# Kernel tuning notes

Hardware: AMD Instinct MI355X
Metric: run time of the kernel (lower is better)

The kernel has to match this reference:

```python
import jax, jax.numpy as jnp
import numpy as np
from jax import lax

B, T, D, H, L = 2048, 512, 64, 16, 10
LOG2PI = float(np.log(2.0 * np.pi))


def _gru_cell(x, h, Wih, Whh, bih, bhh):
    # torch GRUCell gate order: r, z, n
    gi = x @ Wih.T + bih
    gh = h @ Whh.T + bhh
    ir, iz, inn = jnp.split(gi, 3, axis=-1)
    hr, hz, hn = jnp.split(gh, 3, axis=-1)
    r = jax.nn.sigmoid(ir + hr)
    z = jax.nn.sigmoid(iz + hz)
    n = jnp.tanh(inn + r * hn)
    return (1.0 - z) * n + z * h


def _mlp_head(h, W1, b1, W2, b2, Wmu, bmu, Wcov, bcov):
    hh = jax.nn.relu(h @ W1.T + b1)
    hh = jax.nn.relu(hh @ W2.T + b2)
    mu = hh @ Wmu.T + bmu
    sigma = jnp.exp(hh @ Wcov.T + bcov)
    return mu, sigma


def setup_inputs():
    key = jax.random.key(0)
    ks = jax.random.split(key, 24)

    def he(k, shape, fan_in):
        return jax.random.normal(k, shape, dtype=jnp.float32) * np.float32(np.sqrt(2.0 / fan_in))

    z = lambda *s: jnp.zeros(s, jnp.float32)
    p = {}
    p['x'] = jax.random.normal(ks[0], (B, T, D), dtype=jnp.float32)
    p['eps'] = jax.random.normal(ks[1], (B, T, L), dtype=jnp.float32)
    # bidirectional inference GRU
    p['bi_Wih_f'] = he(ks[2], (3 * H, D), D); p['bi_Whh_f'] = he(ks[3], (3 * H, H), H)
    p['bi_bih_f'] = z(3 * H); p['bi_bhh_f'] = z(3 * H)
    p['bi_Wih_b'] = he(ks[4], (3 * H, D), D); p['bi_Whh_b'] = he(ks[5], (3 * H, H), H)
    p['bi_bih_b'] = z(3 * H); p['bi_bhh_b'] = z(3 * H)
    # inference GRUCell on [z_prev, context]
    p['infz_Wih'] = he(ks[6], (3 * H, L + 2 * H), L + 2 * H); p['infz_Whh'] = he(ks[7], (3 * H, H), H)
    p['infz_bih'] = z(3 * H); p['infz_bhh'] = z(3 * H)
    # inference MLP
    p['inf_W1'] = he(ks[8], (H, H), H); p['inf_b1'] = z(H)
    p['inf_W2'] = he(ks[9], (H, H), H); p['inf_b2'] = z(H)
    p['inf_Wmu'] = he(ks[10], (L, H), H); p['inf_bmu'] = z(L)
    p['inf_Wcov'] = he(ks[11], (L, H), H); p['inf_bcov'] = z(L)
    # generative prior GRUCell + MLP (frozen in torch)
    p['genz_Wih'] = he(ks[12], (3 * H, L), L); p['genz_Whh'] = he(ks[13], (3 * H, H), H)
    p['genz_bih'] = z(3 * H); p['genz_bhh'] = z(3 * H)
    p['genzmlp_W1'] = he(ks[14], (H, H), H); p['genzmlp_b1'] = z(H)
    p['genzmlp_W2'] = he(ks[15], (H, H), H); p['genzmlp_b2'] = z(H)
    p['genzmlp_Wmu'] = he(ks[16], (L, H), H); p['genzmlp_bmu'] = z(L)
    p['genzmlp_Wcov'] = he(ks[17], (L, H), H); p['genzmlp_bcov'] = z(L)
    # generative emission GRUCell + MLP (outputs 3*D)
    p['genr_Wih'] = he(ks[18], (3 * H, L), L); p['genr_Whh'] = he(ks[19], (3 * H, H), H)
    p['genr_bih'] = z(3 * H); p['genr_bhh'] = z(3 * H)
    p['genr_W1'] = he(ks[20], (H, H), H); p['genr_b1'] = z(H)
    p['genr_W2'] = he(ks[21], (3 * D, H), H); p['genr_b2'] = z(3 * D)
    return p


def _forward(x, eps, bi_Wih_f, bi_Whh_f, bi_bih_f, bi_bhh_f, bi_Wih_b, bi_Whh_b, bi_bih_b, bi_bhh_b,
             infz_Wih, infz_Whh, infz_bih, infz_bhh,
             inf_W1, inf_b1, inf_W2, inf_b2, inf_Wmu, inf_bmu, inf_Wcov, inf_bcov,
             genz_Wih, genz_Whh, genz_bih, genz_bhh,
             genzmlp_W1, genzmlp_b1, genzmlp_W2, genzmlp_b2, genzmlp_Wmu, genzmlp_bmu, genzmlp_Wcov, genzmlp_bcov,
             genr_Wih, genr_Whh, genr_bih, genr_bhh, genr_W1, genr_b1, genr_W2, genr_b2):
    b, t, d = x.shape
    xt = jnp.transpose(x, (1, 0, 2))      # [T, B, D] time-major
    eps_t = jnp.transpose(eps, (1, 0, 2))  # [T, B, L]
    h0 = jnp.zeros((b, H), x.dtype)

    def fstep(h, xin):
        h2 = _gru_cell(xin, h, bi_Wih_f, bi_Whh_f, bi_bih_f, bi_bhh_f)
        return h2, h2

    def bstep(h, xin):
        h2 = _gru_cell(xin, h, bi_Wih_b, bi_Whh_b, bi_bih_b, bi_bhh_b)
        return h2, h2

    _, fwd = lax.scan(fstep, h0, xt)               # [T, B, H]
    _, bwd_rev = lax.scan(bstep, h0, xt[::-1])
    bwd = bwd_rev[::-1]                            # [T, B, H]

    pad = jnp.zeros((1, b, H), x.dtype)
    h_right = jnp.concatenate([pad, fwd[:-1]], axis=0)   # h^{->}_{t-1}
    h_left = jnp.concatenate([bwd[1:], pad], axis=0)     # h^{<-}_{t+1}
    ctx = jnp.concatenate([h_right, h_left], axis=-1)    # [T, B, 2H]

    def step(carry, inp):
        h_z, h_gz, h_gr, z_prev = carry
        c, e, xi = inp
        h_z = _gru_cell(jnp.concatenate([z_prev, c], axis=-1), h_z, infz_Wih, infz_Whh, infz_bih, infz_bhh)
        q_mu, q_sig = _mlp_head(h_z, inf_W1, inf_b1, inf_W2, inf_b2, inf_Wmu, inf_bmu, inf_Wcov, inf_bcov)
        h_gz = _gru_cell(z_prev, h_gz, genz_Wih, genz_Whh, genz_bih, genz_bhh)
        p_mu, p_sig = _mlp_head(h_gz, genzmlp_W1, genzmlp_b1, genzmlp_W2, genzmlp_b2, genzmlp_Wmu, genzmlp_bmu, genzmlp_Wcov, genzmlp_bcov)
        # KL(N(q_mu,q_sig) || N(p_mu,p_sig))
        kl = jnp.log(p_sig / q_sig) + (q_sig * q_sig + (q_mu - p_mu) ** 2) / (2.0 * p_sig * p_sig) - 0.5
        kl_t = kl.sum(axis=-1).mean()
        z_t = q_mu + q_sig * e  # rsample
        h_gr = _gru_cell(z_t, h_gr, genr_Wih, genr_Whh, genr_bih, genr_bhh)
        r = jax.nn.relu(h_gr @ genr_W1.T + genr_b1) @ genr_W2.T + genr_b2  # [B, 3D]
        r_mu = r[:, :d]
        r_diag = jnp.exp(r[:, d:2 * d]) + 1e-4
        w = r[:, 2 * d:]  # rank-1 cov factor
        # LowRankMVN log_prob via Woodbury (rank 1): Cov = D + w w^T
        delta = xi - r_mu
        dinv = 1.0 / r_diag
        wd = w * dinv
        cap = 1.0 + jnp.sum(wd * w, axis=-1)  # capacitance
        maha = jnp.sum(delta * delta * dinv, axis=-1) - jnp.sum(wd * delta, axis=-1) ** 2 / cap
        logdet = jnp.sum(jnp.log(r_diag), axis=-1) + jnp.log(cap)
        logp = -0.5 * (d * LOG2PI + logdet + maha)
        nll_t = -logp.mean()
        return (h_z, h_gz, h_gr, z_t), (kl_t, nll_t)

    z0 = jnp.zeros((b, L), x.dtype)
    carry0 = (h0, h0, h0, z0)
    _, (kls, nlls) = lax.scan(step, carry0, (ctx, eps_t, xt))
    return nlls.sum(), kls.sum()


def reference(x, eps, bi_Wih_f, bi_Whh_f, bi_bih_f, bi_bhh_f, bi_Wih_b, bi_Whh_b, bi_bih_b, bi_bhh_b,
              infz_Wih, infz_Whh, infz_bih, infz_bhh,
              inf_W1, inf_b1, inf_W2, inf_b2, inf_Wmu, inf_bmu, inf_Wcov, inf_bcov,
              genz_Wih, genz_Whh, genz_bih, genz_bhh,
              genzmlp_W1, genzmlp_b1, genzmlp_W2, genzmlp_b2, genzmlp_Wmu, genzmlp_bmu, genzmlp_Wcov, genzmlp_bcov,
              genr_Wih, genr_Whh, genr_bih, genr_bhh, genr_W1, genr_b1, genr_W2, genr_b2):
    return _forward(x, eps, bi_Wih_f, bi_Whh_f, bi_bih_f, bi_bhh_f, bi_Wih_b, bi_Whh_b, bi_bih_b, bi_bhh_b,
                    infz_Wih, infz_Whh, infz_bih, infz_bhh,
                    inf_W1, inf_b1, inf_W2, inf_b2, inf_Wmu, inf_bmu, inf_Wcov, inf_bcov,
                    genz_Wih, genz_Whh, genz_bih, genz_bhh,
                    genzmlp_W1, genzmlp_b1, genzmlp_W2, genzmlp_b2, genzmlp_Wmu, genzmlp_bmu, genzmlp_Wcov, genzmlp_bcov,
                    genr_Wih, genr_Whh, genr_bih, genr_bhh, genr_W1, genr_b1, genr_W2, genr_b2)
```

## Files before the change

### kernel.cpp

```cpp
#include <hip/hip_runtime.h>

namespace {

typedef __attribute__((ext_vector_type(4))) _Float16 half4v;
typedef __attribute__((ext_vector_type(4))) float   float4v;
typedef unsigned int u32;

#define MFMA16(a,b,c) __builtin_amdgcn_mfma_f32_16x16x16f16((a),(b),(c),0,0,0)

constexpr int Bb = 2048;
constexpr int Tt = 512;
constexpr float LOG2PI_ = 1.8378770664093453f;

struct InPtrs { const float* p[42]; };

__device__ __forceinline__ float rcpf(float x){ return __builtin_amdgcn_rcpf(x); }
__device__ __forceinline__ float sigm(float x){ return rcpf(1.0f + __expf(-x)); }
__device__ __forceinline__ float tanh_(float x){ return 1.0f - 2.0f*rcpf(1.0f + __expf(2.0f*x)); }

__device__ __forceinline__ void barrier_lds(){
  asm volatile("s_waitcnt lgkmcnt(0)" ::: "memory");
  __builtin_amdgcn_s_barrier();
  asm volatile("" ::: "memory");
}

__global__ void zero2(float* out){ if (threadIdx.x < 2) out[threadIdx.x] = 0.f; }

__device__ __forceinline__ void gru_update(const float4v& Dr, const float4v& Dz,
                                           const float4v& Dn, const float4v& Dh, half4v& hB){
  #pragma unroll
  for (int i = 0; i < 4; ++i){
    const float rr = sigm(Dr[i]);
    const float zz = sigm(Dz[i]);
    const float nn = tanh_(Dn[i] + rr*Dh[i]);
    const float hp = (float)hB[i];
    hB[i] = (_Float16)(nn + zz*(hp - nn));
  }
}

__device__ __forceinline__ half4v relu_pack(const float4v& D){
  half4v o;
  #pragma unroll
  for (int i = 0; i < 4; ++i) o[i] = (_Float16)fmaxf(D[i], 0.f);
  return o;
}

constexpr int CH = 8;
constexpr int NCH = Tt / CH;

__global__ __launch_bounds__(128,1) void bigru(InPtrs ip, _Float16* __restrict__ hf,
                                               _Float16* __restrict__ hb)
{
  const int tid = threadIdx.x;
  const int w = tid >> 6;
  const int l = tid & 63, r = l & 15, q = l >> 4;
  const int dir = blockIdx.y;
  const int base = blockIdx.x * 16;

  const float* __restrict__ x   = ip.p[0];
  const float* __restrict__ Wih = dir ? ip.p[6] : ip.p[2];
  const float* __restrict__ Whh = dir ? ip.p[7] : ip.p[3];
  const float* __restrict__ bih = dir ? ip.p[8] : ip.p[4];
  const float* __restrict__ bhh = dir ? ip.p[9] : ip.p[5];
  _Float16* __restrict__ hout = dir ? hb : hf;

  __shared__ __align__(16) float giS[2][CH][64][12];

  half4v Wi[3][4];
  float  b0[4], b1[4], b2[4];
  float4v xp[CH][4];
  half4v Wh[3];
  float  bh2[4];
  half4v hB = {0,0,0,0};
  const float* xrow = x + (size_t)(base + r) * Tt * 64;

  if (w == 1){
    #pragma unroll
    for (int rt = 0; rt < 3; ++rt)
      #pragma unroll
      for (int kt = 0; kt < 4; ++kt)
        #pragma unroll
        for (int j = 0; j < 4; ++j)
          Wi[rt][kt][j] = (_Float16)Wih[(rt*16 + r)*64 + kt*16 + q*4 + j];
    #pragma unroll
    for (int i = 0; i < 4; ++i){
      const int row = q*4 + i;
      b0[i] = bih[row]      + bhh[row];
      b1[i] = bih[16 + row] + bhh[16 + row];
      b2[i] = bih[32 + row];
    }
    #pragma unroll
    for (int s = 0; s < CH; ++s){
      const int tn = dir ? Tt-1-s : s;
      #pragma unroll
      for (int kt = 0; kt < 4; ++kt)
        xp[s][kt] = *(const float4v*)(xrow + (size_t)tn*64 + kt*16 + q*4);
    }
  } else {
    #pragma unroll
    for (int rt = 0; rt < 3; ++rt)
      #pragma unroll
      for (int j = 0; j < 4; ++j)
        Wh[rt][j] = (_Float16)Whh[(rt*16 + r)*16 + q*4 + j];
    #pragma unroll
    for (int i = 0; i < 4; ++i) bh2[i] = bhh[32 + q*4 + i];
  }

  for (int c = 0; c < NCH; ++c){
    if (w == 1){
      #pragma unroll
      for (int st = 0; st < CH; ++st){
        const int tg = c*CH + st;
        half4v xB[4];
        #pragma unroll
        for (int kt = 0; kt < 4; ++kt)
          #pragma unroll
          for (int j = 0; j < 4; ++j) xB[kt][j] = (_Float16)xp[st][kt][j];
        const int tp = tg + CH;
        if (tp < Tt){
          const int tn = dir ? Tt-1-tp : tp;
          #pragma unroll
          for (int kt = 0; kt < 4; ++kt)
            xp[st][kt] = *(const float4v*)(xrow + (size_t)tn*64 + kt*16 + q*4);
        }
        float4v A0 = {b0[0],b0[1],b0[2],b0[3]};
        float4v A1 = {b1[0],b1[1],b1[2],b1[3]};
        float4v A2 = {b2[0],b2[1],b2[2],b2[3]};
        #pragma unroll
        for (int kt = 0; kt < 4; ++kt){
          A0 = MFMA16(Wi[0][kt], xB[kt], A0);
          A1 = MFMA16(Wi[1][kt], xB[kt], A1);
          A2 = MFMA16(Wi[2][kt], xB[kt], A2);
        }
        float* o = &giS[c&1][st][l][0];
        *(float4v*)(o + 0) = A0;
        *(float4v*)(o + 4) = A1;
        *(float4v*)(o + 8) = A2;
      }
    }
    barrier_lds();
    if (w == 0){
      #pragma unroll
      for (int st = 0; st < CH; ++st){
        const int tg = c*CH + st;
        const int t = dir ? Tt-1-tg : tg;
        const float* gi = &giS[c&1][st][l][0];
        float4v A0 = *(const float4v*)(gi + 0);
        float4v A1 = *(const float4v*)(gi + 4);
        float4v A2 = *(const float4v*)(gi + 8);
        float4v Dh = {bh2[0],bh2[1],bh2[2],bh2[3]};
        A0 = MFMA16(Wh[0], hB, A0);
        A1 = MFMA16(Wh[1], hB, A1);
        Dh = MFMA16(Wh[2], hB, Dh);
        gru_update(A0, A1, A2, Dh, hB);
        *(half4v*)(hout + (((size_t)t*Bb + base + r) << 4) + q*4) = hB;
      }
    }
  }
}

__global__ __launch_bounds__(192,1) void vae_seq(InPtrs ip, const _Float16* __restrict__ hf,
                                                 const _Float16* __restrict__ hb,
                                                 _Float16* __restrict__ hz,
                                                 _Float16* __restrict__ hgz,
                                                 _Float16* __restrict__ hgr)
{
  const int tid = threadIdx.x;
  const int w = tid / 64;
  const int l = tid & 63, r = l & 15, q = l >> 4;
  const int base = blockIdx.x * 16;
  const int row0 = q*4;

  __shared__ u32 zS[3][2][64];
  for (int i = tid; i < 3*2*64; i += 192) ((u32*)zS)[i] = 0u;
  barrier_lds();

  half4v WizA[3][3], WhzA[3], I1A, I2A, IMuA, ICovA;
  float bz0[4], bz1[4], bzn[4], bzh[4], bI1v[4], bI2v[4], bIMu[4], bICov[4];
  half4v hzB = {0,0,0,0}, zB = {0,0,0,0};
  half4v hrR[4], hlR[4];
  float4v eR[4];
  half4v WgzA[3], WhgzA[3];
  float bg0[4], bg1[4], bgn[4], bgh[4];
  half4v hgzB = {0,0,0,0};
  half4v WgrA[3], WhgrA[3];
  float br0[4], br1[4], brn[4], brh[4];
  half4v hgrB = {0,0,0,0};

  const float* erow = ip.p[1] + (size_t)(base + r) * Tt * 10;

  if (w == 0){
    #pragma unroll
    for (int rt = 0; rt < 3; ++rt)
      #pragma unroll
      for (int kt = 0; kt < 3; ++kt)
        #pragma unroll
        for (int j = 0; j < 4; ++j){
          const int k = kt*16 + q*4 + j;
          int c;
          if (kt == 0) c = (k < 10) ? k : -1;
          else if (kt == 1) c = 10 + (k - 16);
          else c = 26 + (k - 32);
          WizA[rt][kt][j] = (c >= 0) ? (_Float16)ip.p[10][(rt*16 + r)*42 + c] : (_Float16)0.f;
        }
    #pragma unroll
    for (int rt = 0; rt < 3; ++rt)
      #pragma unroll
      for (int j = 0; j < 4; ++j)
        WhzA[rt][j] = (_Float16)ip.p[11][(rt*16 + r)*16 + q*4 + j];
    #pragma unroll
    for (int j = 0; j < 4; ++j){
      const int k = q*4 + j;
      I1A[j]  = (_Float16)ip.p[14][r*16 + k];
      I2A[j]  = (_Float16)ip.p[16][r*16 + k];
      IMuA[j] = (r < 10) ? (_Float16)ip.p[18][r*16 + k] : (_Float16)0.f;
      ICovA[j]= (r < 10) ? (_Float16)ip.p[20][r*16 + k] : (_Float16)0.f;
    }
    #pragma unroll
    for (int i = 0; i < 4; ++i){
      const int row = row0 + i;
      bz0[i] = ip.p[12][row]    + ip.p[13][row];
      bz1[i] = ip.p[12][16+row] + ip.p[13][16+row];
      bzn[i] = ip.p[12][32+row];
      bzh[i] = ip.p[13][32+row];
      bI1v[i] = ip.p[15][row];  bI2v[i] = ip.p[17][row];
      bIMu[i]  = (row < 10) ? ip.p[19][row] : 0.f;
      bICov[i] = (row < 10) ? ip.p[21][row] : 0.f;
    }
    #pragma unroll
    for (int s = 0; s < 4; ++s){
      if (s >= 1) hrR[s] = *(const half4v*)(hf + (((size_t)(s-1)*Bb + base + r) << 4) + q*4);
      else { half4v z0 = {0,0,0,0}; hrR[s] = z0; }
      hlR[s] = *(const half4v*)(hb + (((size_t)(s+1)*Bb + base + r) << 4) + q*4);
      float4v et;
      #pragma unroll
      for (int ii = 0; ii < 4; ++ii) et[ii] = (row0 + ii < 10) ? erow[s*10 + row0 + ii] : 0.f;
      eR[s] = et;
    }
  } else if (w == 1){
    #pragma unroll
    for (int rt = 0; rt < 3; ++rt)
      #pragma unroll
      for (int j = 0; j < 4; ++j){
        const int k = q*4 + j;
        WgzA[rt][j]  = (k < 10) ? (_Float16)ip.p[22][(rt*16 + r)*10 + k] : (_Float16)0.f;
        WhgzA[rt][j] = (_Float16)ip.p[23][(rt*16 + r)*16 + k];
      }
    #pragma unroll
    for (int i = 0; i < 4; ++i){
      const int row = row0 + i;
      bg0[i] = ip.p[24][row]    + ip.p[25][row];
      bg1[i] = ip.p[24][16+row] + ip.p[25][16+row];
      bgn[i] = ip.p[24][32+row];
      bgh[i] = ip.p[25][32+row];
    }
  } else {
    #pragma unroll
    for (int rt = 0; rt < 3; ++rt)
      #pragma unroll
      for (int j = 0; j < 4; ++j){
        const int k = q*4 + j;
        WgrA[rt][j]  = (k < 10) ? (_Float16)ip.p[34][(rt*16 + r)*10 + k] : (_Float16)0.f;
        WhgrA[rt][j] = (_Float16)ip.p[35][(rt*16 + r)*16 + k];
      }
    #pragma unroll
    for (int i = 0; i < 4; ++i){
      const int row = row0 + i;
      br0[i] = ip.p[36][row]    + ip.p[37][row];
      br1[i] = ip.p[36][16+row] + ip.p[37][16+row];
      brn[i] = ip.p[36][32+row];
      brh[i] = ip.p[37][32+row];
    }
  }

  for (int ib = 0; ib < Tt + 4; ib += 4){
    #pragma unroll
    for (int k = 0; k < 4; ++k){
      const int i = ib + k;
      if (w == 0){
        if (i < Tt){
          const half4v hrB = hrR[k], hlB = hlR[k];
          const float4v ev = eR[k];
          const int f = i + 4;
          if (f < Tt){
            hrR[k] = *(const half4v*)(hf + (((size_t)(f-1)*Bb + base + r) << 4) + q*4);
            if (f <= Tt-2) hlR[k] = *(const half4v*)(hb + (((size_t)(f+1)*Bb + base + r) << 4) + q*4);
            else { half4v z0 = {0,0,0,0}; hlR[k] = z0; }
            float4v et;
            #pragma unroll
            for (int ii = 0; ii < 4; ++ii) et[ii] = (row0 + ii < 10) ? erow[f*10 + row0 + ii] : 0.f;
            eR[k] = et;
          }
          float4v Dr = {bz0[0],bz0[1],bz0[2],bz0[3]};
          float4v Dz = {bz1[0],bz1[1],bz1[2],bz1[3]};
          float4v Dn = {bzn[0],bzn[1],bzn[2],bzn[3]};
          float4v Dh = {bzh[0],bzh[1],bzh[2],bzh[3]};
          Dr = MFMA16(WizA[0][1], hrB, Dr); Dr = MFMA16(WizA[0][2], hlB, Dr);
          Dz = MFMA16(WizA[1][1], hrB, Dz); Dz = MFMA16(WizA[1][2], hlB, Dz);
          Dn = MFMA16(WizA[2][1], hrB, Dn); Dn = MFMA16(WizA[2][2], hlB, Dn);
          Dr = MFMA16(WhzA[0], hzB, Dr);
          Dz = MFMA16(WhzA[1], hzB, Dz);
          Dh = MFMA16(WhzA[2], hzB, Dh);
          Dr = MFMA16(WizA[0][0], zB, Dr);
          Dz = MFMA16(WizA[1][0], zB, Dz);
          Dn = MFMA16(WizA[2][0], zB, Dn);
          gru_update(Dr, Dz, Dn, Dh, hzB);
          *(half4v*)(hz + (((size_t)i*Bb + base + r) << 4) + q*4) = hzB;

          float4v H1 = {bI1v[0],bI1v[1],bI1v[2],bI1v[3]};
          H1 = MFMA16(I1A, hzB, H1);
          const half4v h1B = relu_pack(H1);
          float4v H2 = {bI2v[0],bI2v[1],bI2v[2],bI2v[3]};
          H2 = MFMA16(I2A, h1B, H2);
          const half4v h2B = relu_pack(H2);
          float4v Qmu  = {bIMu[0],bIMu[1],bIMu[2],bIMu[3]};
          float4v Qpre = {bICov[0],bICov[1],bICov[2],bICov[3]};
          Qmu  = MFMA16(IMuA,  h2B, Qmu);
          Qpre = MFMA16(ICovA, h2B, Qpre);

          const int slot = i % 3;
          #pragma unroll
          for (int ii = 0; ii < 4; ++ii){
            const float qs = __expf(Qpre[ii]);
            zB[ii] = (_Float16)(Qmu[ii] + qs*ev[ii]);
          }
          union { half4v h; u32 u[2]; } zc; zc.h = zB;
          zS[slot][0][l] = zc.u[0];
          zS[slot][1][l] = zc.u[1];
        }
      } else if (w == 1){
        if (i >= 1 && i <= Tt){
          const int s = i - 1;
          const int sp = (s - 1 + 3) % 3;
          union { half4v h; u32 u[2]; } zc;
          zc.u[0] = zS[sp][0][l]; zc.u[1] = zS[sp][1][l];
          const half4v zPrev = zc.h;

          float4v Er = {bg0[0],bg0[1],bg0[2],bg0[3]};
          float4v Ez = {bg1[0],bg1[1],bg1[2],bg1[3]};
          float4v En = {bgn[0],bgn[1],bgn[2],bgn[3]};
          float4v Eh = {bgh[0],bgh[1],bgh[2],bgh[3]};
          Er = MFMA16(WgzA[0], zPrev, Er); Er = MFMA16(WhgzA[0], hgzB, Er);
          Ez = MFMA16(WgzA[1], zPrev, Ez); Ez = MFMA16(WhgzA[1], hgzB, Ez);
          En = MFMA16(WgzA[2], zPrev, En);
          Eh = MFMA16(WhgzA[2], hgzB, Eh);
          gru_update(Er, Ez, En, Eh, hgzB);
          *(half4v*)(hgz + (((size_t)s*Bb + base + r) << 4) + q*4) = hgzB;
        }
      } else {
        if (i >= 2 && i < Tt + 2){
          const int u = i - 2;
          union { half4v h; u32 uu[2]; } zc;
          zc.uu[0] = zS[u % 3][0][l]; zc.uu[1] = zS[u % 3][1][l];
          const half4v zU = zc.h;

          float4v Fr = {br0[0],br0[1],br0[2],br0[3]};
          float4v Fz = {br1[0],br1[1],br1[2],br1[3]};
          float4v Fn = {brn[0],brn[1],brn[2],brn[3]};
          float4v Fh = {brh[0],brh[1],brh[2],brh[3]};
          Fr = MFMA16(WgrA[0], zU, Fr); Fr = MFMA16(WhgrA[0], hgrB, Fr);
          Fz = MFMA16(WgrA[1], zU, Fz); Fz = MFMA16(WhgrA[1], hgrB, Fz);
          Fn = MFMA16(WgrA[2], zU, Fn);
          Fh = MFMA16(WhgrA[2], hgrB, Fh);
          gru_update(Fr, Fz, Fn, Fh, hgrB);
          *(half4v*)(hgr + (((size_t)u*Bb + base + r) << 4) + q*4) = hgrB;
        }
      }
      barrier_lds();
    }
  }
}

__global__ __launch_bounds__(256,2) void epi(InPtrs ip, const _Float16* __restrict__ hz,
                                             const _Float16* __restrict__ hgz,
                                             const _Float16* __restrict__ hgr,
                                             float* __restrict__ out)
{
  const int tid = threadIdx.x;
  const int l = tid & 63, r = l & 15, q = l >> 4;
  const int row0 = q*4;

  if (blockIdx.x < 1024){
    const int wid = blockIdx.x * 4 + (tid >> 6);
    const int u0 = wid * 16;

    half4v I1A, I2A, IMuA, ICovA, Z1A, Z2A, ZMuA, ZCovA;
    float bI1v[4], bI2v[4], bIMu[4], bICov[4], bZ1v[4], bZ2v[4], bZMu[4], bZCov[4];
    #pragma unroll
    for (int j = 0; j < 4; ++j){
      const int k = q*4 + j;
      I1A[j]  = (_Float16)ip.p[14][r*16 + k];
      I2A[j]  = (_Float16)ip.p[16][r*16 + k];
      IMuA[j] = (r < 10) ? (_Float16)ip.p[18][r*16 + k] : (_Float16)0.f;
      ICovA[j]= (r < 10) ? (_Float16)ip.p[20][r*16 + k] : (_Float16)0.f;
      Z1A[j]  = (_Float16)ip.p[26][r*16 + k];
      Z2A[j]  = (_Float16)ip.p[28][r*16 + k];
      ZMuA[j] = (r < 10) ? (_Float16)ip.p[30][r*16 + k] : (_Float16)0.f;
      ZCovA[j]= (r < 10) ? (_Float16)ip.p[32][r*16 + k] : (_Float16)0.f;
    }
    #pragma unroll
    for (int i = 0; i < 4; ++i){
      const int row = row0 + i;
      bI1v[i] = ip.p[15][row];  bI2v[i] = ip.p[17][row];
      bIMu[i]  = (row < 10) ? ip.p[19][row] : 0.f;
      bICov[i] = (row < 10) ? ip.p[21][row] : 0.f;
      bZ1v[i] = ip.p[27][row];  bZ2v[i] = ip.p[29][row];
      bZMu[i]  = (row < 10) ? ip.p[31][row] : 0.f;
      bZCov[i] = (row < 10) ? ip.p[33][row] : 0.f;
    }

    float kl_acc = 0.f;
    for (int k = 0; k < 16; ++k){
      const int u = u0 + k;
      const int tile = u >> 9, t = u & 511;
      const size_t off = (((size_t)t*Bb + tile*16 + r) << 4) + q*4;
      const half4v hzB  = *(const half4v*)(hz  + off);
      const half4v hgzB = *(const half4v*)(hgz + off);

      float4v H1 = {bI1v[0],bI1v[1],bI1v[2],bI1v[3]};
      H1 = MFMA16(I1A, hzB, H1);
      const half4v h1B = relu_pack(H1);
      float4v H2 = {bI2v[0],bI2v[1],bI2v[2],bI2v[3]};
      H2 = MFMA16(I2A, h1B, H2);
      const half4v h2B = relu_pack(H2);
      float4v Qmu  = {bIMu[0],bIMu[1],bIMu[2],bIMu[3]};
      float4v Qpre = {bICov[0],bICov[1],bICov[2],bICov[3]};
      Qmu  = MFMA16(IMuA,  h2B, Qmu);
      Qpre = MFMA16(ICovA, h2B, Qpre);

      float4v G1 = {bZ1v[0],bZ1v[1],bZ1v[2],bZ1v[3]};
      G1 = MFMA16(Z1A, hgzB, G1);
      const half4v g1B = relu_pack(G1);
      float4v G2 = {bZ2v[0],bZ2v[1],bZ2v[2],bZ2v[3]};
      G2 = MFMA16(Z2A, g1B, G2);
      const half4v g2B = relu_pack(G2);
      float4v Pmu  = {bZMu[0],bZMu[1],bZMu[2],bZMu[3]};
      float4v Ppre = {bZCov[0],bZCov[1],bZCov[2],bZCov[3]};
      Pmu  = MFMA16(ZMuA,  g2B, Pmu);
      Ppre = MFMA16(ZCovA, g2B, Ppre);

      #pragma unroll
      for (int ii = 0; ii < 4; ++ii){
        const float qs = __expf(Qpre[ii]);
        const float dm = Qmu[ii] - Pmu[ii];
        kl_acc += (Ppre[ii] - Qpre[ii]) + (qs*qs + dm*dm)*0.5f*__expf(-2.f*Ppre[ii]) - 0.5f;
      }
    }
    #pragma unroll
    for (int m = 1; m < 64; m <<= 1) kl_acc += __shfl_xor(kl_acc, m, 64);
    if (l == 0) atomicAdd(&out[1], kl_acc * (1.f/(float)Bb));
  } else {
    const int wid = (blockIdx.x - 1024) * 4 + (tid >> 6);
    const int u0 = wid * 16;

    half4v R1A, R2A[12];
    float bR1v[4], bR2v[12][4];
    #pragma unroll
    for (int j = 0; j < 4; ++j){
      const int k = q*4 + j;
      R1A[j] = (_Float16)ip.p[38][r*16 + k];
      #pragma unroll
      for (int m = 0; m < 12; ++m)
        R2A[m][j] = (_Float16)ip.p[40][(m*16 + r)*16 + k];
    }
    #pragma unroll
    for (int i = 0; i < 4; ++i){
      const int row = row0 + i;
      bR1v[i] = ip.p[39][row];
      #pragma unroll
      for (int m = 0; m < 12; ++m) bR2v[m][i] = ip.p[41][m*16 + row];
    }

    float nll_acc = 0.f;
    for (int k = 0; k < 16; ++k){
      const int u = u0 + k;
      const int tile = u >> 9, t = u & 511;
      const half4v hgrB = *(const half4v*)(hgr + (((size_t)t*Bb + tile*16 + r) << 4) + q*4);
      const float* xrow = ip.p[0] + ((size_t)(tile*16 + r) * Tt + t) * 64;
      float4v xv[4];
      #pragma unroll
      for (int m = 0; m < 4; ++m) xv[m] = *(const float4v*)(xrow + m*16 + q*4);

      float4v R1D = {bR1v[0],bR1v[1],bR1v[2],bR1v[3]};
      R1D = MFMA16(R1A, hgrB, R1D);
      const half4v r1B = relu_pack(R1D);

      float s1 = 0.f, s2 = 0.f, s3 = 0.f, s4 = 0.f;
      #pragma unroll
      for (int m = 0; m < 4; ++m){
        float4v Dmu = {bR2v[m][0],bR2v[m][1],bR2v[m][2],bR2v[m][3]};
        float4v Ddp = {bR2v[4+m][0],bR2v[4+m][1],bR2v[4+m][2],bR2v[4+m][3]};
        float4v Dw  = {bR2v[8+m][0],bR2v[8+m][1],bR2v[8+m][2],bR2v[8+m][3]};
        Dmu = MFMA16(R2A[m],   r1B, Dmu);
        Ddp = MFMA16(R2A[4+m], r1B, Ddp);
        Dw  = MFMA16(R2A[8+m], r1B, Dw);
        #pragma unroll
        for (int ii = 0; ii < 4; ++ii){
          const float diag = __expf(Ddp[ii]) + 1e-4f;
          const float dinv = rcpf(diag);
          const float delta = xv[m][ii] - Dmu[ii];
          const float wv = Dw[ii];
          s1 += delta*delta*dinv;
          s2 += wv*wv*dinv;
          s3 += wv*dinv*delta;
          s4 += __logf(diag);
        }
      }
      s1 += __shfl_xor(s1, 16, 64); s1 += __shfl_xor(s1, 32, 64);
      s2 += __shfl_xor(s2, 16, 64); s2 += __shfl_xor(s2, 32, 64);
      s3 += __shfl_xor(s3, 16, 64); s3 += __shfl_xor(s3, 32, 64);
      s4 += __shfl_xor(s4, 16, 64); s4 += __shfl_xor(s4, 32, 64);
      const float cap = 1.f + s2;
      const float maha = s1 - s3*s3*rcpf(cap);
      const float logdet = s4 + __logf(cap);
      nll_acc += 0.5f*(64.f*LOG2PI_ + logdet + maha);
    }
    #pragma unroll
    for (int m = 1; m < 64; m <<= 1) nll_acc += __shfl_xor(nll_acc, m, 64);
    if (l == 0) atomicAdd(&out[0], nll_acc * 0.25f * (1.f/(float)Bb));
  }
}

}

extern "C" void kernel_launch(void* const* d_in, const int* in_sizes, int n_in,
                              void* d_out, int out_size, void* d_ws, size_t ws_size,
                              hipStream_t stream)
{
  InPtrs ip;
  for (int i = 0; i < 42; ++i) ip.p[i] = (const float*)d_in[i];
  float* out = (float*)d_out;

  const size_t SZ = (size_t)Tt * Bb * 16;
  _Float16* hf  = (_Float16*)d_ws;
  _Float16* hb  = hf  + SZ;
  _Float16* hz  = hb  + SZ;
  _Float16* hgz = hz  + SZ;
  _Float16* hgr = hgz + SZ;

  zero2<<<1, 64, 0, stream>>>(out);
  dim3 gb(Bb/16, 2);
  bigru<<<gb, 128, 0, stream>>>(ip, hf, hb);
  vae_seq<<<Bb/16, 192, 0, stream>>>(ip, hf, hb, hz, hgz, hgr);
  epi<<<2048, 256, 0, stream>>>(ip, hz, hgz, hgr, out);
}
```

Measured before the change: 1.029 ms.

## Collapse warp-specialized GRU kernels into single-wave blocks without LDS barriers

Both the bidirectional GRU and the sequential VAE kernel drop their multi-wave producer/consumer split, in which waves handed data through LDS and synchronised with a block barrier every step. Each block is now a single wave that computes the input projection, the recurrent update, and, for the VAE, all three GRU chains inline per timestep, keeping z in registers. MFMA chains are split into two independent accumulators to shorten dependency latency. This removes per-step barriers and LDS traffic, but each wave now executes more serial work per step with less overlap across waves.

```diff
diff --git a/kernel.cpp b/kernel.cpp
--- a/kernel.cpp
+++ b/kernel.cpp
@@ -17,12 +17,6 @@
 __device__ __forceinline__ float rcpf(float x){ return __builtin_amdgcn_rcpf(x); }
 __device__ __forceinline__ float sigm(float x){ return rcpf(1.0f + __expf(-x)); }
 __device__ __forceinline__ float tanh_(float x){ return 1.0f - 2.0f*rcpf(1.0f + __expf(2.0f*x)); }
-
-__device__ __forceinline__ void barrier_lds(){
-  asm volatile("s_waitcnt lgkmcnt(0)" ::: "memory");
-  __builtin_amdgcn_s_barrier();
-  asm volatile("" ::: "memory");
-}
 
 __global__ void zero2(float* out){ if (threadIdx.x < 2) out[threadIdx.x] = 0.f; }
 
@@ -45,15 +39,10 @@
   return o;
 }
 
-constexpr int CH = 8;
-constexpr int NCH = Tt / CH;
-
-__global__ __launch_bounds__(128,1) void bigru(InPtrs ip, _Float16* __restrict__ hf,
-                                               _Float16* __restrict__ hb)
+__global__ __launch_bounds__(64,1) void bigru(InPtrs ip, _Float16* __restrict__ hf,
+                                              _Float16* __restrict__ hb)
 {
-  const int tid = threadIdx.x;
-  const int w = tid >> 6;
-  const int l = tid & 63, r = l & 15, q = l >> 4;
+  const int l = threadIdx.x & 63, r = l & 15, q = l >> 4;
   const int dir = blockIdx.y;
   const int base = blockIdx.x * 16;
 
@@ -64,309 +53,239 @@
   const float* __restrict__ bhh = dir ? ip.p[9] : ip.p[5];
   _Float16* __restrict__ hout = dir ? hb : hf;
 
-  __shared__ __align__(16) float giS[2][CH][64][12];
-
-  half4v Wi[3][4];
-  float  b0[4], b1[4], b2[4];
-  float4v xp[CH][4];
-  half4v Wh[3];
-  float  bh2[4];
+  half4v Wi[3][4], Wh[3];
+  float  b0[4], b1[4], b2[4], bh2[4];
+  float4v xp[4][4];
   half4v hB = {0,0,0,0};
   const float* xrow = x + (size_t)(base + r) * Tt * 64;
 
-  if (w == 1){
-    #pragma unroll
-    for (int rt = 0; rt < 3; ++rt)
+  #pragma unroll
+  for (int rt = 0; rt < 3; ++rt)
+    #pragma unroll
+    for (int kt = 0; kt < 4; ++kt)
+      #pragma unroll
+      for (int j = 0; j < 4; ++j)
+        Wi[rt][kt][j] = (_Float16)Wih[(rt*16 + r)*64 + kt*16 + q*4 + j];
+  #pragma unroll
+  for (int rt = 0; rt < 3; ++rt)
+    #pragma unroll
+    for (int j = 0; j < 4; ++j)
+      Wh[rt][j] = (_Float16)Whh[(rt*16 + r)*16 + q*4 + j];
+  #pragma unroll
+  for (int i = 0; i < 4; ++i){
+    const int row = q*4 + i;
+    b0[i] = bih[row]      + bhh[row];
+    b1[i] = bih[16 + row] + bhh[16 + row];
+    b2[i] = bih[32 + row];
+    bh2[i] = bhh[32 + row];
+  }
+  #pragma unroll
+  for (int s = 0; s < 4; ++s){
+    const int tn = dir ? Tt-1-s : s;
+    #pragma unroll
+    for (int kt = 0; kt < 4; ++kt)
+      xp[s][kt] = *(const float4v*)(xrow + (size_t)tn*64 + kt*16 + q*4);
+  }
+
+  for (int ib = 0; ib < Tt; ib += 4){
+    #pragma unroll
+    for (int k = 0; k < 4; ++k){
+      const int tg = ib + k;
+      const int t = dir ? Tt-1-tg : tg;
+      half4v xB[4];
       #pragma unroll
       for (int kt = 0; kt < 4; ++kt)
         #pragma unroll
-        for (int j = 0; j < 4; ++j)
-          Wi[rt][kt][j] = (_Float16)Wih[(rt*16 + r)*64 + kt*16 + q*4 + j];
-    #pragma unroll
-    for (int i = 0; i < 4; ++i){
-      const int row = q*4 + i;
-      b0[i] = bih[row]      + bhh[row];
-      b1[i] = bih[16 + row] + bhh[16 + row];
-      b2[i] = bih[32 + row];
-    }
-    #pragma unroll
-    for (int s = 0; s < CH; ++s){
-      const int tn = dir ? Tt-1-s : s;
-      #pragma unroll
-      for (int kt = 0; kt < 4; ++kt)
-        xp[s][kt] = *(const float4v*)(xrow + (size_t)tn*64 + kt*16 + q*4);
-    }
-  } else {
-    #pragma unroll
-    for (int rt = 0; rt < 3; ++rt)
-      #pragma unroll
-      for (int j = 0; j < 4; ++j)
-        Wh[rt][j] = (_Float16)Whh[(rt*16 + r)*16 + q*4 + j];
-    #pragma unroll
-    for (int i = 0; i < 4; ++i) bh2[i] = bhh[32 + q*4 + i];
-  }
-
-  for (int c = 0; c < NCH; ++c){
-    if (w == 1){
-      #pragma unroll
-      for (int st = 0; st < CH; ++st){
-        const int tg = c*CH + st;
-        half4v xB[4];
+        for (int j = 0; j < 4; ++j) xB[kt][j] = (_Float16)xp[k][kt][j];
+      const int tp = tg + 4;
+      if (tp < Tt){
+        const int tn = dir ? Tt-1-tp : tp;
         #pragma unroll
         for (int kt = 0; kt < 4; ++kt)
-          #pragma unroll
-          for (int j = 0; j < 4; ++j) xB[kt][j] = (_Float16)xp[st][kt][j];
-        const int tp = tg + CH;
-        if (tp < Tt){
-          const int tn = dir ? Tt-1-tp : tp;
-          #pragma unroll
-          for (int kt = 0; kt < 4; ++kt)
-            xp[st][kt] = *(const float4v*)(xrow + (size_t)tn*64 + kt*16 + q*4);
-        }
-        float4v A0 = {b0[0],b0[1],b0[2],b0[3]};
-        float4v A1 = {b1[0],b1[1],b1[2],b1[3]};
-        float4v A2 = {b2[0],b2[1],b2[2],b2[3]};
-        #pragma unroll
-        for (int kt = 0; kt < 4; ++kt){
-          A0 = MFMA16(Wi[0][kt], xB[kt], A0);
-          A1 = MFMA16(Wi[1][kt], xB[kt], A1);
-          A2 = MFMA16(Wi[2][kt], xB[kt], A2);
-        }
-        float* o = &giS[c&1][st][l][0];
-        *(float4v*)(o + 0) = A0;
-        *(float4v*)(o + 4) = A1;
-        *(float4v*)(o + 8) = A2;
+          xp[k][kt] = *(const float4v*)(xrow + (size_t)tn*64 + kt*16 + q*4);
       }
-    }
-    barrier_lds();
-    if (w == 0){
-      #pragma unroll
-      for (int st = 0; st < CH; ++st){
-        const int tg = c*CH + st;
-        const int t = dir ? Tt-1-tg : tg;
-        const float* gi = &giS[c&1][st][l][0];
-        float4v A0 = *(const float4v*)(gi + 0);
-        float4v A1 = *(const float4v*)(gi + 4);
-        float4v A2 = *(const float4v*)(gi + 8);
-        float4v Dh = {bh2[0],bh2[1],bh2[2],bh2[3]};
-        A0 = MFMA16(Wh[0], hB, A0);
-        A1 = MFMA16(Wh[1], hB, A1);
-        Dh = MFMA16(Wh[2], hB, Dh);
-        gru_update(A0, A1, A2, Dh, hB);
-        *(half4v*)(hout + (((size_t)t*Bb + base + r) << 4) + q*4) = hB;
-      }
-    }
-  }
-}
-
-__global__ __launch_bounds__(192,1) void vae_seq(InPtrs ip, const _Float16* __restrict__ hf,
-                                                 const _Float16* __restrict__ hb,
-                                                 _Float16* __restrict__ hz,
-                                                 _Float16* __restrict__ hgz,
-                                                 _Float16* __restrict__ hgr)
+      float4v A0 = {b0[0],b0[1],b0[2],b0[3]};
+      float4v A1 = {b1[0],b1[1],b1[2],b1[3]};
+      float4v A2 = {b2[0],b2[1],b2[2],b2[3]};
+      float4v A0x = {0,0,0,0}, A1x = {0,0,0,0}, A2x = {0,0,0,0};
+      A0 = MFMA16(Wi[0][0], xB[0], A0); A0 = MFMA16(Wi[0][1], xB[1], A0);
+      A1 = MFMA16(Wi[1][0], xB[0], A1); A1 = MFMA16(Wi[1][1], xB[1], A1);
+      A2 = MFMA16(Wi[2][0], xB[0], A2); A2 = MFMA16(Wi[2][1], xB[1], A2);
+      A0x = MFMA16(Wi[0][2], xB[2], A0x); A0x = MFMA16(Wi[0][3], xB[3], A0x);
+      A1x = MFMA16(Wi[1][2], xB[2], A1x); A1x = MFMA16(Wi[1][3], xB[3], A1x);
+      A2x = MFMA16(Wi[2][2], xB[2], A2x); A2x = MFMA16(Wi[2][3], xB[3], A2x);
+      #pragma unroll
+      for (int ii = 0; ii < 4; ++ii){ A0[ii] += A0x[ii]; A1[ii] += A1x[ii]; A2[ii] += A2x[ii]; }
+      float4v Dh = {bh2[0],bh2[1],bh2[2],bh2[3]};
+      A0 = MFMA16(Wh[0], hB, A0);
+      A1 = MFMA16(Wh[1], hB, A1);
+      Dh = MFMA16(Wh[2], hB, Dh);
+      gru_update(A0, A1, A2, Dh, hB);
+      *(half4v*)(hout + (((size_t)t*Bb + base + r) << 4) + q*4) = hB;
+    }
+  }
+}
+
+__global__ __launch_bounds__(64,1) void vae_fused(InPtrs ip, const _Float16* __restrict__ hf,
+                                                  const _Float16* __restrict__ hb,
+                                                  _Float16* __restrict__ hz,
+                                                  _Float16* __restrict__ hgz,
+                                                  _Float16* __restrict__ hgr)
 {
-  const int tid = threadIdx.x;
-  const int w = tid / 64;
-  const int l = tid & 63, r = l & 15, q = l >> 4;
+  const int l = threadIdx.x & 63, r = l & 15, q = l >> 4;
   const int base = blockIdx.x * 16;
   const int row0 = q*4;
 
-  __shared__ u32 zS[3][2][64];
-  for (int i = tid; i < 3*2*64; i += 192) ((u32*)zS)[i] = 0u;
-  barrier_lds();
-
   half4v WizA[3][3], WhzA[3], I1A, I2A, IMuA, ICovA;
   float bz0[4], bz1[4], bzn[4], bzh[4], bI1v[4], bI2v[4], bIMu[4], bICov[4];
-  half4v hzB = {0,0,0,0}, zB = {0,0,0,0};
+  half4v WgzA[3], WhgzA[3];
+  float bg0[4], bg1[4], bgn[4], bgh[4];
+  half4v WgrA[3], WhgrA[3];
+  float br0[4], br1[4], brn[4], brh[4];
+  half4v hzB = {0,0,0,0}, hgzB = {0,0,0,0}, hgrB = {0,0,0,0}, zB = {0,0,0,0};
   half4v hrR[4], hlR[4];
   float4v eR[4];
-  half4v WgzA[3], WhgzA[3];
-  float bg0[4], bg1[4], bgn[4], bgh[4];
-  half4v hgzB = {0,0,0,0};
-  half4v WgrA[3], WhgrA[3];
-  float br0[4], br1[4], brn[4], brh[4];
-  half4v hgrB = {0,0,0,0};
 
   const float* erow = ip.p[1] + (size_t)(base + r) * Tt * 10;
-
-  if (w == 0){
-    #pragma unroll
-    for (int rt = 0; rt < 3; ++rt)
-      #pragma unroll
-      for (int kt = 0; kt < 3; ++kt)
-        #pragma unroll
-        for (int j = 0; j < 4; ++j){
-          const int k = kt*16 + q*4 + j;
-          int c;
-          if (kt == 0) c = (k < 10) ? k : -1;
-          else if (kt == 1) c = 10 + (k - 16);
-          else c = 26 + (k - 32);
-          WizA[rt][kt][j] = (c >= 0) ? (_Float16)ip.p[10][(rt*16 + r)*42 + c] : (_Float16)0.f;
-        }
-    #pragma unroll
-    for (int rt = 0; rt < 3; ++rt)
-      #pragma unroll
-      for (int j = 0; j < 4; ++j)
-        WhzA[rt][j] = (_Float16)ip.p[11][(rt*16 + r)*16 + q*4 + j];
+  int eo[4];
+  #pragma unroll
+  for (int ii = 0; ii < 4; ++ii) eo[ii] = (row0 + ii < 10) ? (row0 + ii) : 9;
+
+  #pragma unroll
+  for (int rt = 0; rt < 3; ++rt)
+    #pragma unroll
+    for (int kt = 0; kt < 3; ++kt)
+      #pragma unroll
+      for (int j = 0; j < 4; ++j){
+        const int k = kt*16 + q*4 + j;
+        int c;
+        if (kt == 0) c = (k < 10) ? k : -1;
+        else if (kt == 1) c = 10 + (k - 16);
+        else c = 26 + (k - 32);
+        WizA[rt][kt][j] = (c >= 0) ? (_Float16)ip.p[10][(rt*16 + r)*42 + c] : (_Float16)0.f;
+      }
+  #pragma unroll
+  for (int rt = 0; rt < 3; ++rt)
     #pragma unroll
     for (int j = 0; j < 4; ++j){
       const int k = q*4 + j;
-      I1A[j]  = (_Float16)ip.p[14][r*16 + k];
-      I2A[j]  = (_Float16)ip.p[16][r*16 + k];
-      IMuA[j] = (r < 10) ? (_Float16)ip.p[18][r*16 + k] : (_Float16)0.f;
-      ICovA[j]= (r < 10) ? (_Float16)ip.p[20][r*16 + k] : (_Float16)0.f;
-    }
-    #pragma unroll
-    for (int i = 0; i < 4; ++i){
-      const int row = row0 + i;
-      bz0[i] = ip.p[12][row]    + ip.p[13][row];
-      bz1[i] = ip.p[12][16+row] + ip.p[13][16+row];
-      bzn[i] = ip.p[12][32+row];
-      bzh[i] = ip.p[13][32+row];
-      bI1v[i] = ip.p[15][row];  bI2v[i] = ip.p[17][row];
-      bIMu[i]  = (row < 10) ? ip.p[19][row] : 0.f;
-      bICov[i] = (row < 10) ? ip.p[21][row] : 0.f;
-    }
-    #pragma unroll
-    for (int s = 0; s < 4; ++s){
-      if (s >= 1) hrR[s] = *(const half4v*)(hf + (((size_t)(s-1)*Bb + base + r) << 4) + q*4);
-      else { half4v z0 = {0,0,0,0}; hrR[s] = z0; }
-      hlR[s] = *(const half4v*)(hb + (((size_t)(s+1)*Bb + base + r) << 4) + q*4);
-      float4v et;
-      #pragma unroll
-      for (int ii = 0; ii < 4; ++ii) et[ii] = (row0 + ii < 10) ? erow[s*10 + row0 + ii] : 0.f;
-      eR[s] = et;
-    }
-  } else if (w == 1){
-    #pragma unroll
-    for (int rt = 0; rt < 3; ++rt)
-      #pragma unroll
-      for (int j = 0; j < 4; ++j){
-        const int k = q*4 + j;
-        WgzA[rt][j]  = (k < 10) ? (_Float16)ip.p[22][(rt*16 + r)*10 + k] : (_Float16)0.f;
-        WhgzA[rt][j] = (_Float16)ip.p[23][(rt*16 + r)*16 + k];
-      }
-    #pragma unroll
-    for (int i = 0; i < 4; ++i){
-      const int row = row0 + i;
-      bg0[i] = ip.p[24][row]    + ip.p[25][row];
-      bg1[i] = ip.p[24][16+row] + ip.p[25][16+row];
-      bgn[i] = ip.p[24][32+row];
-      bgh[i] = ip.p[25][32+row];
-    }
-  } else {
-    #pragma unroll
-    for (int rt = 0; rt < 3; ++rt)
-      #pragma unroll
-      for (int j = 0; j < 4; ++j){
-        const int k = q*4 + j;
-        WgrA[rt][j]  = (k < 10) ? (_Float16)ip.p[34][(rt*16 + r)*10 + k] : (_Float16)0.f;
-        WhgrA[rt][j] = (_Float16)ip.p[35][(rt*16 + r)*16 + k];
-      }
-    #pragma unroll
-    for (int i = 0; i < 4; ++i){
-      const int row = row0 + i;
-      br0[i] = ip.p[36][row]    + ip.p[37][row];
-      br1[i] = ip.p[36][16+row] + ip.p[37][16+row];
-      brn[i] = ip.p[36][32+row];
-      brh[i] = ip.p[37][32+row];
-    }
-  }
-
-  for (int ib = 0; ib < Tt + 4; ib += 4){
+      WhzA[rt][j]  = (_Float16)ip.p[11][(rt*16 + r)*16 + k];
+      WgzA[rt][j]  = (k < 10) ? (_Float16)ip.p[22][(rt*16 + r)*10 + k] : (_Float16)0.f;
+      WhgzA[rt][j] = (_Float16)ip.p[23][(rt*16 + r)*16 + k];
+      WgrA[rt][j]  = (k < 10) ? (_Float16)ip.p[34][(rt*16 + r)*10 + k] : (_Float16)0.f;
+      WhgrA[rt][j] = (_Float16)ip.p[35][(rt*16 + r)*16 + k];
+    }
+  #pragma unroll
+  for (int j = 0; j < 4; ++j){
+    const int k = q*4 + j;
+    I1A[j]  = (_Float16)ip.p[14][r*16 + k];
+    I2A[j]  = (_Float16)ip.p[16][r*16 + k];
+    IMuA[j] = (r < 10) ? (_Float16)ip.p[18][r*16 + k] : (_Float16)0.f;
+    ICovA[j]= (r < 10) ? (_Float16)ip.p[20][r*16 + k] : (_Float16)0.f;
+  }
+  #pragma unroll
+  for (int i = 0; i < 4; ++i){
+    const int row = row0 + i;
+    bz0[i] = ip.p[12][row]    + ip.p[13][row];
+    bz1[i] = ip.p[12][16+row] + ip.p[13][16+row];
+    bzn[i] = ip.p[12][32+row];
+    bzh[i] = ip.p[13][32+row];
+    bI1v[i] = ip.p[15][row];  bI2v[i] = ip.p[17][row];
+    bIMu[i]  = (row < 10) ? ip.p[19][row] : 0.f;
+    bICov[i] = (row < 10) ? ip.p[21][row] : 0.f;
+    bg0[i] = ip.p[24][row]    + ip.p[25][row];
+    bg1[i] = ip.p[24][16+row] + ip.p[25][16+row];
+    bgn[i] = ip.p[24][32+row];
+    bgh[i] = ip.p[25][32+row];
+    br0[i] = ip.p[36][row]    + ip.p[37][row];
+    br1[i] = ip.p[36][16+row] + ip.p[37][16+row];
+    brn[i] = ip.p[36][32+row];
+    brh[i] = ip.p[37][32+row];
+  }
+  #pragma unroll
+  for (int s = 0; s < 4; ++s){
+    if (s >= 1) hrR[s] = *(const half4v*)(hf + (((size_t)(s-1)*Bb + base + r) << 4) + q*4);
+    else { half4v z0 = {0,0,0,0}; hrR[s] = z0; }
+    hlR[s] = *(const half4v*)(hb + (((size_t)(s+1)*Bb + base + r) << 4) + q*4);
+    float4v et;
+    #pragma unroll
+    for (int ii = 0; ii < 4; ++ii) et[ii] = erow[s*10 + eo[ii]];
+    eR[s] = et;
+  }
+
+  for (int ib = 0; ib < Tt; ib += 4){
     #pragma unroll
     for (int k = 0; k < 4; ++k){
       const int i = ib + k;
-      if (w == 0){
-        if (i < Tt){
-          const half4v hrB = hrR[k], hlB = hlR[k];
-          const float4v ev = eR[k];
-          const int f = i + 4;
-          if (f < Tt){
-            hrR[k] = *(const half4v*)(hf + (((size_t)(f-1)*Bb + base + r) << 4) + q*4);
-            if (f <= Tt-2) hlR[k] = *(const half4v*)(hb + (((size_t)(f+1)*Bb + base + r) << 4) + q*4);
-            else { half4v z0 = {0,0,0,0}; hlR[k] = z0; }
-            float4v et;
-            #pragma unroll
-            for (int ii = 0; ii < 4; ++ii) et[ii] = (row0 + ii < 10) ? erow[f*10 + row0 + ii] : 0.f;
-            eR[k] = et;
-          }
-          float4v Dr = {bz0[0],bz0[1],bz0[2],bz0[3]};
-          float4v Dz = {bz1[0],bz1[1],bz1[2],bz1[3]};
-          float4v Dn = {bzn[0],bzn[1],bzn[2],bzn[3]};
-          float4v Dh = {bzh[0],bzh[1],bzh[2],bzh[3]};
-          Dr = MFMA16(WizA[0][1], hrB, Dr); Dr = MFMA16(WizA[0][2], hlB, Dr);
-          Dz = MFMA16(WizA[1][1], hrB, Dz); Dz = MFMA16(WizA[1][2], hlB, Dz);
-          Dn = MFMA16(WizA[2][1], hrB, Dn); Dn = MFMA16(WizA[2][2], hlB, Dn);
-          Dr = MFMA16(WhzA[0], hzB, Dr);
-          Dz = MFMA16(WhzA[1], hzB, Dz);
-          Dh = MFMA16(WhzA[2], hzB, Dh);
-          Dr = MFMA16(WizA[0][0], zB, Dr);
-          Dz = MFMA16(WizA[1][0], zB, Dz);
-          Dn = MFMA16(WizA[2][0], zB, Dn);
-          gru_update(Dr, Dz, Dn, Dh, hzB);
-          *(half4v*)(hz + (((size_t)i*Bb + base + r) << 4) + q*4) = hzB;
-
-          float4v H1 = {bI1v[0],bI1v[1],bI1v[2],bI1v[3]};
-          H1 = MFMA16(I1A, hzB, H1);
-          const half4v h1B = relu_pack(H1);
-          float4v H2 = {bI2v[0],bI2v[1],bI2v[2],bI2v[3]};
-          H2 = MFMA16(I2A, h1B, H2);
-          const half4v h2B = relu_pack(H2);
-          float4v Qmu  = {bIMu[0],bIMu[1],bIMu[2],bIMu[3]};
-          float4v Qpre = {bICov[0],bICov[1],bICov[2],bICov[3]};
-          Qmu  = MFMA16(IMuA,  h2B, Qmu);
-          Qpre = MFMA16(ICovA, h2B, Qpre);
-
-          const int slot = i % 3;
-          #pragma unroll
-          for (int ii = 0; ii < 4; ++ii){
-            const float qs = __expf(Qpre[ii]);
-            zB[ii] = (_Float16)(Qmu[ii] + qs*ev[ii]);
-          }
-          union { half4v h; u32 u[2]; } zc; zc.h = zB;
-          zS[slot][0][l] = zc.u[0];
-          zS[slot][1][l] = zc.u[1];
-        }
-      } else if (w == 1){
-        if (i >= 1 && i <= Tt){
-          const int s = i - 1;
-          const int sp = (s - 1 + 3) % 3;
-          union { half4v h; u32 u[2]; } zc;
-          zc.u[0] = zS[sp][0][l]; zc.u[1] = zS[sp][1][l];
-          const half4v zPrev = zc.h;
-
-          float4v Er = {bg0[0],bg0[1],bg0[2],bg0[3]};
-          float4v Ez = {bg1[0],bg1[1],bg1[2],bg1[3]};
-          float4v En = {bgn[0],bgn[1],bgn[2],bgn[3]};
-          float4v Eh = {bgh[0],bgh[1],bgh[2],bgh[3]};
-          Er = MFMA16(WgzA[0], zPrev, Er); Er = MFMA16(WhgzA[0], hgzB, Er);
-          Ez = MFMA16(WgzA[1], zPrev, Ez); Ez = MFMA16(WhgzA[1], hgzB, Ez);
-          En = MFMA16(WgzA[2], zPrev, En);
-          Eh = MFMA16(WhgzA[2], hgzB, Eh);
-          gru_update(Er, Ez, En, Eh, hgzB);
-          *(half4v*)(hgz + (((size_t)s*Bb + base + r) << 4) + q*4) = hgzB;
-        }
-      } else {
-        if (i >= 2 && i < Tt + 2){
-          const int u = i - 2;
-          union { half4v h; u32 uu[2]; } zc;
-          zc.uu[0] = zS[u % 3][0][l]; zc.uu[1] = zS[u % 3][1][l];
-          const half4v zU = zc.h;
-
-          float4v Fr = {br0[0],br0[1],br0[2],br0[3]};
-          float4v Fz = {br1[0],br1[1],br1[2],br1[3]};
-          float4v Fn = {brn[0],brn[1],brn[2],brn[3]};
-          float4v Fh = {brh[0],brh[1],brh[2],brh[3]};
-          Fr = MFMA16(WgrA[0], zU, Fr); Fr = MFMA16(WhgrA[0], hgrB, Fr);
-          Fz = MFMA16(WgrA[1], zU, Fz); Fz = MFMA16(WhgrA[1], hgrB, Fz);
-          Fn = MFMA16(WgrA[2], zU, Fn);
-          Fh = MFMA16(WhgrA[2], hgrB, Fh);
-          gru_update(Fr, Fz, Fn, Fh, hgrB);
-          *(half4v*)(hgr + (((size_t)u*Bb + base + r) << 4) + q*4) = hgrB;
-        }
+      const half4v hrB = hrR[k], hlB = hlR[k];
+      const float4v ev = eR[k];
+      const int f = i + 4;
+      if (f < Tt){
+        hrR[k] = *(const half4v*)(hf + (((size_t)(f-1)*Bb + base + r) << 4) + q*4);
+        if (f <= Tt-2) hlR[k] = *(const half4v*)(hb + (((size_t)(f+1)*Bb + base + r) << 4) + q*4);
+        else { half4v z0 = {0,0,0,0}; hlR[k] = z0; }
+        float4v et;
+        #pragma unroll
+        for (int ii = 0; ii < 4; ++ii) et[ii] = erow[f*10 + eo[ii]];
+        eR[k] = et;
       }
-      barrier_lds();
+
+      float4v Er = {bg0[0],bg0[1],bg0[2],bg0[3]};
+      float4v Ez = {bg1[0],bg1[1],bg1[2],bg1[3]};
+      float4v En = {bgn[0],bgn[1],bgn[2],bgn[3]};
+      float4v Eh = {bgh[0],bgh[1],bgh[2],bgh[3]};
+      Er = MFMA16(WgzA[0], zB, Er); Er = MFMA16(WhgzA[0], hgzB, Er);
+      Ez = MFMA16(WgzA[1], zB, Ez); Ez = MFMA16(WhgzA[1], hgzB, Ez);
+      En = MFMA16(WgzA[2], zB, En);
+      Eh = MFMA16(WhgzA[2], hgzB, Eh);
+
+      float4v Dr = {bz0[0],bz0[1],bz0[2],bz0[3]};
+      float4v Dz = {bz1[0],bz1[1],bz1[2],bz1[3]};
+      float4v Dn = {bzn[0],bzn[1],bzn[2],bzn[3]};
+      float4v Dh = {bzh[0],bzh[1],bzh[2],bzh[3]};
+      float4v DrX = {0,0,0,0}, DzX = {0,0,0,0}, DnX = {0,0,0,0};
+      Dr = MFMA16(WizA[0][1], hrB, Dr); Dr = MFMA16(WhzA[0], hzB, Dr);
+      Dz = MFMA16(WizA[1][1], hrB, Dz); Dz = MFMA16(WhzA[1], hzB, Dz);
+      Dn = MFMA16(WizA[2][1], hrB, Dn); Dn = MFMA16(WizA[2][2], hlB, Dn);
+      DrX = MFMA16(WizA[0][2], hlB, DrX); DrX = MFMA16(WizA[0][0], zB, DrX);
+      DzX = MFMA16(WizA[1][2], hlB, DzX); DzX = MFMA16(WizA[1][0], zB, DzX);
+      DnX = MFMA16(WizA[2][0], zB, DnX);
+      Dh = MFMA16(WhzA[2], hzB, Dh);
+      #pragma unroll
+      for (int ii = 0; ii < 4; ++ii){ Dr[ii] += DrX[ii]; Dz[ii] += DzX[ii]; Dn[ii] += DnX[ii]; }
+      gru_update(Dr, Dz, Dn, Dh, hzB);
+      *(half4v*)(hz + (((size_t)i*Bb + base + r) << 4) + q*4) = hzB;
+
+      gru_update(Er, Ez, En, Eh, hgzB);
+      *(half4v*)(hgz + (((size_t)i*Bb + base + r) << 4) + q*4) = hgzB;
+
+      float4v H1 = {bI1v[0],bI1v[1],bI1v[2],bI1v[3]};
+      H1 = MFMA16(I1A, hzB, H1);
+      const half4v h1B = relu_pack(H1);
+      float4v H2 = {bI2v[0],bI2v[1],bI2v[2],bI2v[3]};
+      H2 = MFMA16(I2A, h1B, H2);
+      const half4v h2B = relu_pack(H2);
+      float4v Qmu  = {bIMu[0],bIMu[1],bIMu[2],bIMu[3]};
+      float4v Qpre = {bICov[0],bICov[1],bICov[2],bICov[3]};
+      Qmu  = MFMA16(IMuA,  h2B, Qmu);
+      Qpre = MFMA16(ICovA, h2B, Qpre);
+      half4v zN;
+      #pragma unroll
+      for (int ii = 0; ii < 4; ++ii)
+        zN[ii] = (_Float16)(Qmu[ii] + __expf(Qpre[ii])*ev[ii]);
+
+      float4v Fr = {br0[0],br0[1],br0[2],br0[3]};
+      float4v Fz = {br1[0],br1[1],br1[2],br1[3]};
+      float4v Fn = {brn[0],brn[1],brn[2],brn[3]};
+      float4v Fh = {brh[0],brh[1],brh[2],brh[3]};
+      Fr = MFMA16(WgrA[0], zN, Fr); Fr = MFMA16(WhgrA[0], hgrB, Fr);
+      Fz = MFMA16(WgrA[1], zN, Fz); Fz = MFMA16(WhgrA[1], hgrB, Fz);
+      Fn = MFMA16(WgrA[2], zN, Fn);
+      Fh = MFMA16(WhgrA[2], hgrB, Fh);
+      gru_update(Fr, Fz, Fn, Fh, hgrB);
+      *(half4v*)(hgr + (((size_t)i*Bb + base + r) << 4) + q*4) = hgrB;
+
+      zB = zN;
     }
   }
 }
@@ -540,7 +459,7 @@
 
   zero2<<<1, 64, 0, stream>>>(out);
   dim3 gb(Bb/16, 2);
-  bigru<<<gb, 128, 0, stream>>>(ip, hf, hb);
-  vae_seq<<<Bb/16, 192, 0, stream>>>(ip, hf, hb, hz, hgz, hgr);
+  bigru<<<gb, 64, 0, stream>>>(ip, hf, hb);
+  vae_fused<<<Bb/16, 64, 0, stream>>>(ip, hf, hb, hz, hgz, hgr);
   epi<<<2048, 256, 0, stream>>>(ip, hz, hgz, hgr, out);
 }
```

Result: slower. 1.327 ms (+28.9%).
